# Optimization experiments

Measured on AMD Instinct MI355X. Metric: run time of the kernel, lower is better.

The kernel has to match this reference:

```python
import jax, jax.numpy as jnp
import numpy as np

B, T, D = 2, 2048, 1024
H = 16
HD = D // H  # head dim == config.k == config.v == 64


def setup_inputs() -> dict:
    key = jax.random.key(0)
    k1, k2, k3 = jax.random.split(key, 3)
    scale = 0.02
    x = jax.random.normal(k1, (B, T, D), dtype=jnp.float32)
    W1 = jax.random.normal(k2, (D, 3 * D), dtype=jnp.float32) * scale
    b1 = jnp.zeros((3 * D,), dtype=jnp.float32)
    W2 = jax.random.normal(k3, (D, D), dtype=jnp.float32) * scale
    b2 = jnp.zeros((D,), dtype=jnp.float32)
    return {"x": x, "W1": W1, "b1": b1, "W2": W2, "b2": b2}


def reference(x, W1, b1, W2, b2):
    # Fused QKV projection (dropout layers are identity in eval mode).
    Bx, Tx, C = x.shape
    qkv = x @ W1 + b1                      # [B, T, 3D]
    q, k, v = jnp.split(qkv, 3, axis=-1)   # each [B, T, D]
    q = q.reshape(Bx, Tx, H, HD).transpose(0, 2, 1, 3)  # [B, H, T, hd]
    k = k.reshape(Bx, Tx, H, HD).transpose(0, 2, 1, 3)
    v = v.reshape(Bx, Tx, H, HD).transpose(0, 2, 1, 3)

    logits = jnp.einsum('bhmk,bhnk->bhmn', q, k) / jnp.sqrt(jnp.float32(HD))
    # causal mask (lower-triangular bias buffer)
    causal = jnp.tril(jnp.ones((Tx, Tx), dtype=bool))
    logits = jnp.where(causal[None, None], logits, jnp.float32(-jnp.inf))
    att = jax.nn.softmax(logits, axis=-1)   # [B, H, T, T]

    y = jnp.einsum('bhmn,bhnv->bhmv', att, v)        # [B, H, T, hd]
    y = y.transpose(0, 2, 1, 3).reshape(Bx, Tx, C)   # [B, T, D]
    return y @ W2 + b2
```

## Files before the change

### kernel.cpp

```cpp
#include <hip/hip_runtime.h>

typedef __attribute__((ext_vector_type(8))) short bf16x8;
typedef __attribute__((ext_vector_type(4))) float f32x4;
typedef __attribute__((ext_vector_type(16))) float f32x16;
typedef __attribute__((ext_vector_type(4))) short short4v;
typedef __attribute__((ext_vector_type(4))) unsigned int uint4v;

#define B_  2
#define T_  2048
#define D_  1024
#define H_  16
#define HD_ 64

__device__ inline short f2bf(float f){
  unsigned u = __builtin_bit_cast(unsigned, f);
  u += 0x7fff + ((u >> 16) & 1);
  return (short)(u >> 16);
}
__device__ inline float bf2f(short s){
  unsigned u = ((unsigned)(unsigned short)s) << 16;
  return __builtin_bit_cast(float, u);
}

__device__ inline void gl2lds16(const void* g, void* l){
  __builtin_amdgcn_global_load_lds(
      (const __attribute__((address_space(1))) unsigned int*)g,
      (__attribute__((address_space(3))) unsigned int*)l, 16, 0, 0);
}

__device__ inline void transpose_tile(const float* __restrict__ in,
                                      short* __restrict__ out,
                                      int R, int C, int bx, int by){
  __shared__ float tile[32][33];
  int tx = threadIdx.x & 31, ty0 = threadIdx.x >> 5;
#pragma unroll
  for (int i = 0; i < 4; i++){
    int ty = ty0 + i * 8;
    tile[ty][tx] = in[(by + ty) * C + bx + tx];
  }
  __syncthreads();
#pragma unroll
  for (int i = 0; i < 4; i++){
    int ty = ty0 + i * 8;
    out[(bx + ty) * R + by + tx] = f2bf(tile[tx][ty]);
  }
}

__global__ __launch_bounds__(256) void prep(
    const float* __restrict__ x,  short* __restrict__ xb,
    const float* __restrict__ W1, short* __restrict__ W1T,
    const float* __restrict__ W2, short* __restrict__ W2T){
  const int bid = blockIdx.x;
  if (bid < 4096){
    int i = (bid * 256 + threadIdx.x) * 4;
    float4 v = *(const float4*)(x + i);
    short4v o;
    o[0] = f2bf(v.x); o[1] = f2bf(v.y); o[2] = f2bf(v.z); o[3] = f2bf(v.w);
    *(short4v*)(xb + i) = o;
  } else if (bid < 4096 + 3072){
    int tb = bid - 4096;
    transpose_tile(W1, W1T, 1024, 3072, (tb % 96) << 5, (tb / 96) << 5);
  } else {
    int tb = bid - 7168;
    transpose_tile(W2, W2T, 1024, 1024, (tb % 32) << 5, (tb / 32) << 5);
  }
}

#define QSCALE 0.18033688011112042f

__global__ __launch_bounds__(512) void gemm_qkv8(
    const short* __restrict__ A, const short* __restrict__ Bt,
    const float* __restrict__ bias,
    short* __restrict__ q, short* __restrict__ kk, short* __restrict__ vT){
  constexpr int K_ = 1024, NT = K_ / 64;
  __shared__ short As[2][256 * 64];
  __shared__ short Bs[2][192 * 64];
  const int tid = threadIdx.x;
  const int lane = tid & 63, w = tid >> 6;
  const int wm = w >> 2, wn = w & 3;
  const int lr = lane & 15, lk = lane >> 4;
  const int brow = blockIdx.y * 256, bcol = blockIdx.x * 192;
  const short* Ag = A  + brow * K_;
  const short* Bg = Bt + bcol * K_;
  f32x4 acc[8][3] = {};

  auto stageA = [&](int buf, int k0, int j){
    int idx = j * 512 + tid;
    int row = idx >> 3, cb = (idx & 7) * 16;
    int cs = cb ^ ((row & 7) << 4);
    gl2lds16(Ag + row * K_ + k0 + (cs >> 1), (char*)As[buf] + idx * 16);
  };
  auto stageB = [&](int buf, int k0, int j){
    int idx = j * 512 + tid;
    int row = idx >> 3, cb = (idx & 7) * 16;
    int cs = cb ^ ((row & 7) << 4);
    gl2lds16(Bg + row * K_ + k0 + (cs >> 1), (char*)Bs[buf] + idx * 16);
  };

#pragma unroll
  for (int j = 0; j < 4; j++) stageA(0, 0, j);
#pragma unroll
  for (int j = 0; j < 3; j++) stageB(0, 0, j);
  asm volatile("s_waitcnt vmcnt(0)" ::: "memory");
  __builtin_amdgcn_s_barrier();
  __builtin_amdgcn_sched_barrier(0);

  for (int t = 0; t < NT; ++t){
    const int cur = t & 1;
    const short* Ac = As[cur];
    const short* Bc = Bs[cur];
    const int nk0 = (t + 1) * 64;
    const bool pf = (t + 1 < NT);
    bf16x8 b[3][2];
#pragma unroll
    for (int p = 0; p < 4; p++){
      if (p == 0){
#pragma unroll
        for (int nf = 0; nf < 3; nf++){
          int rrow = wn * 48 + nf * 16 + lr;
          const char* rp = (const char*)Bc + rrow * 128;
          int swz = (rrow & 7) << 4;
#pragma unroll
          for (int kx = 0; kx < 2; kx++)
            b[nf][kx] = *(const bf16x8*)(rp + ((kx * 64 + lk * 16) ^ swz));
        }
      }
      bf16x8 a[2][2];
#pragma unroll
      for (int mf = 0; mf < 2; mf++){
        int arow = wm * 128 + p * 32 + mf * 16 + lr;
        const char* rp = (const char*)Ac + arow * 128;
        int swz = (arow & 7) << 4;
#pragma unroll
        for (int kx = 0; kx < 2; kx++)
          a[mf][kx] = *(const bf16x8*)(rp + ((kx * 64 + lk * 16) ^ swz));
      }
      if (pf){
        if (p == 0){ stageA(cur ^ 1, nk0, 0); stageA(cur ^ 1, nk0, 1); }
        else if (p == 1){ stageA(cur ^ 1, nk0, 2); stageA(cur ^ 1, nk0, 3); }
        else if (p == 2){ stageB(cur ^ 1, nk0, 0); stageB(cur ^ 1, nk0, 1); }
        else          {  stageB(cur ^ 1, nk0, 2); }
      }
      __builtin_amdgcn_sched_barrier(0);
      __builtin_amdgcn_s_barrier();
      __builtin_amdgcn_sched_barrier(0);
      __builtin_amdgcn_s_setprio(1);
#pragma unroll
      for (int mf = 0; mf < 2; mf++)
#pragma unroll
        for (int nf = 0; nf < 3; nf++)
#pragma unroll
          for (int kx = 0; kx < 2; kx++)
            acc[p * 2 + mf][nf] = __builtin_amdgcn_mfma_f32_16x16x32_bf16(
                a[mf][kx], b[nf][kx], acc[p * 2 + mf][nf], 0, 0, 0);
      __builtin_amdgcn_s_setprio(0);
      __builtin_amdgcn_sched_barrier(0);
      if (p == 3 && pf)
        asm volatile("s_waitcnt vmcnt(0)" ::: "memory");
      __builtin_amdgcn_s_barrier();
      __builtin_amdgcn_sched_barrier(0);
    }
  }

#pragma unroll
  for (int nf = 0; nf < 3; nf++){
    int n = bcol + wn * 48 + nf * 16 + lr;
    float bv = bias[n];
    int sec = n >> 10, d = n & 1023, h = d >> 6, hd = d & 63;
#pragma unroll
    for (int qd = 0; qd < 8; qd++){
      int m0 = brow + wm * 128 + qd * 16 + lk * 4;
      int bb = m0 >> 11, t0 = m0 & 2047;
      int bh = bb * H_ + h;
      if (sec == 0){
#pragma unroll
        for (int r = 0; r < 4; r++)
          q[(bh * T_ + t0 + r) * HD_ + hd] = f2bf((acc[qd][nf][r] + bv) * QSCALE);
      } else if (sec == 1){
#pragma unroll
        for (int r = 0; r < 4; r++)
          kk[(bh * T_ + t0 + r) * HD_ + hd] = f2bf(acc[qd][nf][r] + bv);
      } else {
        float v0 = acc[qd][nf][0] + bv, v1 = acc[qd][nf][1] + bv;
        float v2 = acc[qd][nf][2] + bv, v3 = acc[qd][nf][3] + bv;
        unsigned lo = (unsigned)(unsigned short)f2bf(v0) | ((unsigned)(unsigned short)f2bf(v1) << 16);
        unsigned hi = (unsigned)(unsigned short)f2bf(v2) | ((unsigned)(unsigned short)f2bf(v3) << 16);
        uint2 pk; pk.x = lo; pk.y = hi;
        *(uint2*)(vT + (bh * HD_ + hd) * T_ + t0) = pk;
      }
    }
  }
}

#define BM 128
#define BN 128
#define BK 32

template<int N_, int K_>
__global__ __launch_bounds__(256, 3) void gemm_bt(
    const short* __restrict__ A, const short* __restrict__ Bt,
    const float* __restrict__ bias, float* __restrict__ outf){
  __shared__ short As[3][BM * BK];
  __shared__ short Bs[3][BN * BK];
  const int tid = threadIdx.x;
  const int lane = tid & 63, w = tid >> 6;
  const int wm = w >> 1, wn = w & 1;
  const int lr = lane & 15, lk = lane >> 4;
  const int brow = blockIdx.y * BM, bcol = blockIdx.x * BN;
  f32x4 acc[4][4] = {};
  const short* Ag = A  + brow * K_;
  const short* Bg = Bt + bcol * K_;

  auto stage = [&](int buf, int k0){
#pragma unroll
    for (int i = 0; i < 2; i++){
      int idx = i * 256 + tid;
      int row = idx >> 2, c8 = (idx & 3) * 8;
      gl2lds16(Ag + row * K_ + k0 + c8, (char*)As[buf] + idx * 16);
      gl2lds16(Bg + row * K_ + k0 + c8, (char*)Bs[buf] + idx * 16);
    }
  };

  const int NT = K_ / BK;
  stage(0, 0);
  stage(1, BK);
  for (int t = 0; t < NT; ++t){
    if (t + 1 < NT)
      asm volatile("s_waitcnt vmcnt(4)" ::: "memory");
    else
      asm volatile("s_waitcnt vmcnt(0)" ::: "memory");
    __builtin_amdgcn_s_barrier();
    __builtin_amdgcn_sched_barrier(0);
    if (t + 2 < NT)
      stage((t + 2) % 3, (t + 2) * BK);
    __builtin_amdgcn_sched_barrier(0);

    const short* Ac = As[t % 3];
    const short* Bc = Bs[t % 3];
    bf16x8 a[4], b[4];
#pragma unroll
    for (int mf = 0; mf < 4; mf++)
      a[mf] = *(const bf16x8*)(Ac + (wm * 64 + mf * 16 + lr) * BK + lk * 8);
#pragma unroll
    for (int nf = 0; nf < 4; nf++)
      b[nf] = *(const bf16x8*)(Bc + (wn * 64 + nf * 16 + lr) * BK + lk * 8);
    __builtin_amdgcn_s_setprio(1);
#pragma unroll
    for (int mf = 0; mf < 4; mf++)
#pragma unroll
      for (int nf = 0; nf < 4; nf++)
        acc[mf][nf] = __builtin_amdgcn_mfma_f32_16x16x32_bf16(a[mf], b[nf], acc[mf][nf], 0, 0, 0);
    __builtin_amdgcn_s_setprio(0);
  }

#pragma unroll
  for (int nf = 0; nf < 4; nf++){
    int n = bcol + wn * 64 + nf * 16 + lr;
    float bv = bias[n];
#pragma unroll
    for (int mf = 0; mf < 4; mf++){
      int m0 = brow + wm * 64 + mf * 16 + lk * 4;
#pragma unroll
      for (int r = 0; r < 4; r++)
        outf[(m0 + r) * N_ + n] = acc[mf][nf][r] + bv;
    }
  }
}

__device__ inline int crow(int r, int h){ return (r & 3) + 8 * (r >> 2) + 4 * h; }

template<int NS>
__global__ __launch_bounds__(256, 4) void attn32(
    const short* __restrict__ Q, const short* __restrict__ Kg,
    const short* __restrict__ Vt, short* __restrict__ Y,
    short* __restrict__ Op, float* __restrict__ ml){
  __shared__ short Ks[2][64 * 64];
  __shared__ short Vs[2][64 * 64];
  __shared__ float bounce[4][32];
  const int tid = threadIdx.x;
  const int w = tid >> 6, l = tid & 63;
  const int lq = l & 31, h = l >> 5;
  const int bx = blockIdx.x;
  int i, hf;
  if constexpr (NS == 4){
    int u = bx >> 5, v = u & 15;
    i = (v < 8) ? 15 - v : v - 8;
    hf = u >> 4;
  } else {
    i = (bx < 256) ? 15 - (bx >> 5) : (bx >> 5) - 8;
    hf = 0;
  }
  const int bh = bx & 31;
  const int q0 = i * 128, qw = q0 + w * 32;
  const int nt = 2 * (i + 1);
  const int t0 = hf * nt / NS;
  const int t1 = (hf + 1) * nt / NS;

  bf16x8 qb[4];
  {
    const short* qbase = Q + (bh * T_ + qw + lq) * HD_;
#pragma unroll
    for (int dk = 0; dk < 4; dk++)
      qb[dk] = *(const bf16x8*)(qbase + dk * 16 + h * 8);
  }

  f32x16 o0 = {}, o1 = {};
  float m = -1e30f, ll = 0.f;

  auto stage = [&](int buf, int t){
#pragma unroll
    for (int j = 0; j < 2; j++){
      int idx = j * 256 + tid;
      int row = idx >> 3, cb = (idx & 7) * 16;
      int cbs = cb ^ ((row & 7) << 4);
      gl2lds16(Kg + (bh * T_ + t * 64 + row) * HD_ + (cbs >> 1), (char*)Ks[buf] + idx * 16);
      gl2lds16(Vt + (bh * HD_ + row) * T_ + t * 64 + (cbs >> 1), (char*)Vs[buf] + idx * 16);
    }
  };

  if (t0 < t1){
    stage(0, t0);
    for (int t = t0; t < t1; ++t){
      const int cur = (t - t0) & 1;
      if (t + 1 < t1){
        stage(cur ^ 1, t + 1);
        asm volatile("s_waitcnt vmcnt(4)" ::: "memory");
      } else {
        asm volatile("s_waitcnt vmcnt(0)" ::: "memory");
      }
      __builtin_amdgcn_s_barrier();
      __builtin_amdgcn_sched_barrier(0);

      const int kvb = t * 64;
      if (kvb <= qw + 31){
        const short* Kc = Ks[cur];
        const short* Vc = Vs[cur];

        f32x16 s[2] = {};
        __builtin_amdgcn_s_setprio(1);
#pragma unroll
        for (int kb = 0; kb < 2; kb++){
          int row = kb * 32 + lq;
          const char* rp = (const char*)Kc + row * 128;
          int swz = (row & 7) << 4;
#pragma unroll
          for (int dk = 0; dk < 4; dk++){
            bf16x8 ka = *(const bf16x8*)(rp + ((dk * 32 + h * 16) ^ swz));
            s[kb] = __builtin_amdgcn_mfma_f32_32x32x16_bf16(ka, qb[dk], s[kb], 0, 0, 0);
          }
        }
        __builtin_amdgcn_s_setprio(0);

        const int qg = qw + lq;
        if (kvb + 63 > qw){
#pragma unroll
          for (int kb = 0; kb < 2; kb++)
#pragma unroll
            for (int r = 0; r < 16; r++){
              int kv = kvb + kb * 32 + crow(r, h);
              if (kv > qg) s[kb][r] = -1e30f;
            }
        }

        float pm = s[0][0];
#pragma unroll
        for (int r = 1; r < 16; r++) pm = fmaxf(pm, s[0][r]);
#pragma unroll
        for (int r = 0; r < 16; r++) pm = fmaxf(pm, s[1][r]);
        pm = fmaxf(pm, __shfl_xor(pm, 32));

        if (__any(pm > m + 8.f)){
          float mn = fmaxf(pm, m);
          float sf = __builtin_amdgcn_exp2f(m - mn);
          m = mn;
          ll *= sf;
          bounce[w][lq] = sf;
#pragma unroll
          for (int r = 0; r < 16; r++){
            float sr = bounce[w][crow(r, h)];
            o0[r] *= sr; o1[r] *= sr;
          }
        }

        float ts = 0.f;
#pragma unroll
        for (int kb = 0; kb < 2; kb++)
#pragma unroll
          for (int r = 0; r < 16; r++){
            float p = __builtin_amdgcn_exp2f(s[kb][r] - m);
            s[kb][r] = p;
            ts += p;
          }
        ts += __shfl_xor(ts, 32);
        ll += ts;

        unsigned pw0[8], pw1[8];
#pragma unroll
        for (int kb = 0; kb < 2; kb++)
#pragma unroll
          for (int gg = 0; gg < 4; gg++){
            unsigned r0, r1;
            asm("v_cvt_pk_bf16_f32 %0, %1, %2" : "=v"(r0) : "v"(s[kb][gg * 4 + 0]), "v"(s[kb][gg * 4 + 1]));
            asm("v_cvt_pk_bf16_f32 %0, %1, %2" : "=v"(r1) : "v"(s[kb][gg * 4 + 2]), "v"(s[kb][gg * 4 + 3]));
            pw0[kb * 4 + gg] = r0;
            pw1[kb * 4 + gg] = r1;
          }
#pragma unroll
        for (int ks = 0; ks < 4; ks++){
          asm("v_permlane32_swap_b32 %0, %1" : "+v"(pw0[2 * ks]), "+v"(pw0[2 * ks + 1]));
          asm("v_permlane32_swap_b32 %0, %1" : "+v"(pw1[2 * ks]), "+v"(pw1[2 * ks + 1]));
        }

        __builtin_amdgcn_s_setprio(1);
#pragma unroll
        for (int ks = 0; ks < 4; ks++){
          uint4v paw;
          paw[0] = pw0[2 * ks];     paw[1] = pw1[2 * ks];
          paw[2] = pw0[2 * ks + 1]; paw[3] = pw1[2 * ks + 1];
          bf16x8 pa = __builtin_bit_cast(bf16x8, paw);
#pragma unroll
          for (int nb = 0; nb < 2; nb++){
            int row = nb * 32 + lq;
            bf16x8 vb = *(const bf16x8*)((const char*)Vc + row * 128 +
                          ((ks * 32 + h * 16) ^ ((row & 7) << 4)));
            if (nb == 0) o0 = __builtin_amdgcn_mfma_f32_32x32x16_bf16(pa, vb, o0, 0, 0, 0);
            else         o1 = __builtin_amdgcn_mfma_f32_32x32x16_bf16(pa, vb, o1, 0, 0, 0);
          }
        }
        __builtin_amdgcn_s_setprio(0);
      }
      __builtin_amdgcn_sched_barrier(0);
      __builtin_amdgcn_s_barrier();
    }
  }

  if constexpr (NS == 4){
    short* Oq = Op + ((size_t)(hf * 32 + bh)) * (size_t)T_ * 64;
    if (h == 0){
      float* mlr = ml + ((size_t)(hf * 32 + bh) * T_ + (qw + lq)) * 2;
      mlr[0] = m; mlr[1] = ll;
    }
#pragma unroll
    for (int r = 0; r < 16; r++){
      int qg = qw + crow(r, h);
      Oq[qg * 64 + lq]      = f2bf(o0[r]);
      Oq[qg * 64 + 32 + lq] = f2bf(o1[r]);
    }
  } else {
    bounce[w][lq] = __builtin_amdgcn_rcpf(ll);
    const int b = bh >> 4, hh = bh & 15;
#pragma unroll
    for (int r = 0; r < 16; r++){
      int row = crow(r, h);
      float rl = bounce[w][row];
      int qg = qw + row;
      short* yb = Y + (b * T_ + qg) * D_ + hh * 64;
      yb[lq]      = f2bf(o0[r] * rl);
      yb[32 + lq] = f2bf(o1[r] * rl);
    }
  }
}

__global__ __launch_bounds__(256) void attn_merge(
    const short* __restrict__ Op, const float* __restrict__ ml,
    short* __restrict__ Y){
  int gid = blockIdx.x * 256 + threadIdx.x;
  int rid = gid >> 2, c16 = (gid & 3) * 16;
  float mh[4], lh[4];
#pragma unroll
  for (int hf = 0; hf < 4; hf++){
    float2 v = *(const float2*)(ml + (size_t)hf * 131072 + rid * 2);
    mh[hf] = v.x; lh[hf] = v.y;
  }
  float M = fmaxf(fmaxf(mh[0], mh[1]), fmaxf(mh[2], mh[3]));
  float f[4], den = 0.f;
#pragma unroll
  for (int hf = 0; hf < 4; hf++){
    f[hf] = __builtin_amdgcn_exp2f(mh[hf] - M);
    den += f[hf] * lh[hf];
  }
  float rl = 1.f / den;
  float acc[16] = {};
#pragma unroll
  for (int hf = 0; hf < 4; hf++){
    const short* o = Op + (size_t)hf * 4194304 + (size_t)rid * 64 + c16;
    bf16x8 a = *(const bf16x8*)(o);
    bf16x8 b = *(const bf16x8*)(o + 8);
    float fh = f[hf];
#pragma unroll
    for (int j = 0; j < 8; j++){
      acc[j]     += fh * bf2f(a[j]);
      acc[8 + j] += fh * bf2f(b[j]);
    }
  }
  int bh = rid >> 11, t = rid & 2047;
  short* yb = Y + (((bh >> 4) * T_ + t) * D_) + (bh & 15) * 64 + c16;
  bf16x8 o0, o1;
#pragma unroll
  for (int j = 0; j < 8; j++){
    o0[j] = f2bf(acc[j] * rl);
    o1[j] = f2bf(acc[8 + j] * rl);
  }
  *(bf16x8*)(yb)     = o0;
  *(bf16x8*)(yb + 8) = o1;
}

extern "C" void kernel_launch(void* const* d_in, const int* in_sizes, int n_in,
                              void* d_out, int out_size, void* d_ws, size_t ws_size,
                              hipStream_t stream) {
  const float* x  = (const float*)d_in[0];
  const float* W1 = (const float*)d_in[1];
  const float* b1 = (const float*)d_in[2];
  const float* W2 = (const float*)d_in[3];
  const float* b2 = (const float*)d_in[4];
  float* out = (float*)d_out;

  char* ws = (char*)d_ws;
  short* W1T = (short*)(ws);
  short* W2T = (short*)(ws + 6291456);
  short* xb  = (short*)(ws + 8388608);
  short* q   = (short*)(ws + 16777216);
  short* kk  = (short*)(ws + 25165824);
  short* vT  = (short*)(ws + 33554432);
  short* Op  = (short*)(ws + 41943040);
  float* mlb = (float*)(ws);
  short* y   = xb;

  const size_t need = 41943040ull + 33554432ull;
  const bool split = ws_size >= need;

  prep<<<dim3(8192), dim3(256), 0, stream>>>(x, xb, W1, W1T, W2, W2T);
  gemm_qkv8<<<dim3(16, 16), dim3(512), 0, stream>>>(xb, W1T, b1, q, kk, vT);
  if (split){
    attn32<4><<<dim3(2048), dim3(256), 0, stream>>>(q, kk, vT, nullptr, Op, mlb);
    attn_merge<<<dim3(1024), dim3(256), 0, stream>>>(Op, mlb, y);
  } else {
    attn32<1><<<dim3(512), dim3(256), 0, stream>>>(q, kk, vT, y, nullptr, nullptr);
  }
  gemm_bt<1024, 1024><<<dim3(8, 32), dim3(256), 0, stream>>>(y, W2T, b2, out);
}
```

Baseline: 112.2 us.

## Enlarge QKV GEMM tile to 256x256 with four-phase LDS/MFMA interleaved schedule

The QKV projection GEMM now computes 256x256 output tiles instead of 256x192, dropping the grid from 16x16 to 12x16 blocks and raising arithmetic intensity per LDS load. The main loop is restructured into four quadrant sub-steps that interleave LDS fragment loads and global-to-LDS prefetch of the next K-tile with MFMA bursts, and each wave now stages its own rows. The goal is more data reuse and better overlap of memory with compute. In exchange, LDS use and accumulator registers grow, which may reduce occupancy, and 192 blocks may underfill the 256 CUs.

```diff
diff --git a/kernel.cpp b/kernel.cpp
--- a/kernel.cpp
+++ b/kernel.cpp
@@ -74,97 +74,113 @@
     short* __restrict__ q, short* __restrict__ kk, short* __restrict__ vT){
   constexpr int K_ = 1024, NT = K_ / 64;
   __shared__ short As[2][256 * 64];
-  __shared__ short Bs[2][192 * 64];
+  __shared__ short Bs[2][256 * 64];
   const int tid = threadIdx.x;
   const int lane = tid & 63, w = tid >> 6;
   const int wm = w >> 2, wn = w & 3;
   const int lr = lane & 15, lk = lane >> 4;
-  const int brow = blockIdx.y * 256, bcol = blockIdx.x * 192;
+  const int brow = blockIdx.y * 256, bcol = blockIdx.x * 256;
   const short* Ag = A  + brow * K_;
   const short* Bg = Bt + bcol * K_;
-  f32x4 acc[8][3] = {};
-
-  auto stageA = [&](int buf, int k0, int j){
-    int idx = j * 512 + tid;
-    int row = idx >> 3, cb = (idx & 7) * 16;
-    int cs = cb ^ ((row & 7) << 4);
-    gl2lds16(Ag + row * K_ + k0 + (cs >> 1), (char*)As[buf] + idx * 16);
+  f32x4 acc[8][4] = {};
+
+  auto stageA = [&](int buf, int k0){
+#pragma unroll
+    for (int j = 0; j < 4; j++){
+      int row = wm * 128 + wn * 32 + j * 8 + (lane >> 3);
+      int colb = (lane & 7) * 16;
+      int cs = colb ^ ((row & 7) << 4);
+      gl2lds16(Ag + row * K_ + k0 + (cs >> 1), (char*)As[buf] + row * 128 + colb);
+    }
   };
-  auto stageB = [&](int buf, int k0, int j){
-    int idx = j * 512 + tid;
-    int row = idx >> 3, cb = (idx & 7) * 16;
-    int cs = cb ^ ((row & 7) << 4);
-    gl2lds16(Bg + row * K_ + k0 + (cs >> 1), (char*)Bs[buf] + idx * 16);
+  auto stageB = [&](int buf, int k0){
+#pragma unroll
+    for (int j = 0; j < 4; j++){
+      int row = (wn >> 1) * 128 + (wm * 2 + (wn & 1)) * 32 + j * 8 + (lane >> 3);
+      int colb = (lane & 7) * 16;
+      int cs = colb ^ ((row & 7) << 4);
+      gl2lds16(Bg + row * K_ + k0 + (cs >> 1), (char*)Bs[buf] + row * 128 + colb);
+    }
   };
 
-#pragma unroll
-  for (int j = 0; j < 4; j++) stageA(0, 0, j);
-#pragma unroll
-  for (int j = 0; j < 3; j++) stageB(0, 0, j);
-  asm volatile("s_waitcnt vmcnt(0)" ::: "memory");
-  __builtin_amdgcn_s_barrier();
-  __builtin_amdgcn_sched_barrier(0);
+  bf16x8 aF[8], bF[4], bF2[4];
+  auto loadA = [&](const short* Ac, int r){
+#pragma unroll
+    for (int mf = 0; mf < 4; mf++){
+      int row = wm * 128 + r * 64 + mf * 16 + lr;
+      const char* rp = (const char*)Ac + row * 128;
+      int swz = (row & 7) << 4;
+#pragma unroll
+      for (int kx = 0; kx < 2; kx++)
+        aF[mf * 2 + kx] = *(const bf16x8*)(rp + ((kx * 64 + lk * 16) ^ swz));
+    }
+  };
+  auto loadB = [&](const short* Bc, int c, bf16x8* dst){
+#pragma unroll
+    for (int nf = 0; nf < 2; nf++){
+      int row = wn * 64 + c * 32 + nf * 16 + lr;
+      const char* rp = (const char*)Bc + row * 128;
+      int swz = (row & 7) << 4;
+#pragma unroll
+      for (int kx = 0; kx < 2; kx++)
+        dst[nf * 2 + kx] = *(const bf16x8*)(rp + ((kx * 64 + lk * 16) ^ swz));
+    }
+  };
+
+#define MFMA_SUB(r, c, B)                                                    \
+  __builtin_amdgcn_s_setprio(1);                                             \
+  _Pragma("unroll")                                                          \
+  for (int mf = 0; mf < 4; mf++)                                             \
+    _Pragma("unroll")                                                        \
+    for (int nf = 0; nf < 2; nf++)                                           \
+      _Pragma("unroll")                                                      \
+      for (int kx = 0; kx < 2; kx++)                                         \
+        acc[(r)*4 + mf][(c)*2 + nf] = __builtin_amdgcn_mfma_f32_16x16x32_bf16(\
+            aF[mf*2+kx], (B)[nf*2+kx], acc[(r)*4 + mf][(c)*2 + nf], 0, 0, 0);\
+  __builtin_amdgcn_s_setprio(0);
+
+  stageA(0, 0);
+  stageB(0, 0);
 
   for (int t = 0; t < NT; ++t){
-    const int cur = t & 1;
+    const int cur = t & 1, nxt = cur ^ 1;
     const short* Ac = As[cur];
     const short* Bc = Bs[cur];
-    const int nk0 = (t + 1) * 64;
     const bool pf = (t + 1 < NT);
-    bf16x8 b[3][2];
-#pragma unroll
-    for (int p = 0; p < 4; p++){
-      if (p == 0){
-#pragma unroll
-        for (int nf = 0; nf < 3; nf++){
-          int rrow = wn * 48 + nf * 16 + lr;
-          const char* rp = (const char*)Bc + rrow * 128;
-          int swz = (rrow & 7) << 4;
-#pragma unroll
-          for (int kx = 0; kx < 2; kx++)
-            b[nf][kx] = *(const bf16x8*)(rp + ((kx * 64 + lk * 16) ^ swz));
-        }
-      }
-      bf16x8 a[2][2];
-#pragma unroll
-      for (int mf = 0; mf < 2; mf++){
-        int arow = wm * 128 + p * 32 + mf * 16 + lr;
-        const char* rp = (const char*)Ac + arow * 128;
-        int swz = (arow & 7) << 4;
-#pragma unroll
-        for (int kx = 0; kx < 2; kx++)
-          a[mf][kx] = *(const bf16x8*)(rp + ((kx * 64 + lk * 16) ^ swz));
-      }
-      if (pf){
-        if (p == 0){ stageA(cur ^ 1, nk0, 0); stageA(cur ^ 1, nk0, 1); }
-        else if (p == 1){ stageA(cur ^ 1, nk0, 2); stageA(cur ^ 1, nk0, 3); }
-        else if (p == 2){ stageB(cur ^ 1, nk0, 0); stageB(cur ^ 1, nk0, 1); }
-        else          {  stageB(cur ^ 1, nk0, 2); }
-      }
-      __builtin_amdgcn_sched_barrier(0);
-      __builtin_amdgcn_s_barrier();
-      __builtin_amdgcn_sched_barrier(0);
-      __builtin_amdgcn_s_setprio(1);
-#pragma unroll
-      for (int mf = 0; mf < 2; mf++)
-#pragma unroll
-        for (int nf = 0; nf < 3; nf++)
-#pragma unroll
-          for (int kx = 0; kx < 2; kx++)
-            acc[p * 2 + mf][nf] = __builtin_amdgcn_mfma_f32_16x16x32_bf16(
-                a[mf][kx], b[nf][kx], acc[p * 2 + mf][nf], 0, 0, 0);
-      __builtin_amdgcn_s_setprio(0);
-      __builtin_amdgcn_sched_barrier(0);
-      if (p == 3 && pf)
-        asm volatile("s_waitcnt vmcnt(0)" ::: "memory");
-      __builtin_amdgcn_s_barrier();
-      __builtin_amdgcn_sched_barrier(0);
-    }
-  }
-
-#pragma unroll
-  for (int nf = 0; nf < 3; nf++){
-    int n = bcol + wn * 48 + nf * 16 + lr;
+    asm volatile("s_waitcnt vmcnt(0)" ::: "memory");
+    __builtin_amdgcn_s_barrier();
+    __builtin_amdgcn_sched_barrier(0);
+    loadA(Ac, 0);
+    loadB(Bc, 0, bF);
+    if (pf) stageA(nxt, (t + 1) * 64);
+    __builtin_amdgcn_sched_barrier(0);
+    __builtin_amdgcn_s_barrier();
+    __builtin_amdgcn_sched_barrier(0);
+    MFMA_SUB(0, 0, bF)
+    __builtin_amdgcn_sched_barrier(0);
+    __builtin_amdgcn_s_barrier();
+    loadB(Bc, 1, bF2);
+    if (pf) stageB(nxt, (t + 1) * 64);
+    __builtin_amdgcn_sched_barrier(0);
+    __builtin_amdgcn_s_barrier();
+    __builtin_amdgcn_sched_barrier(0);
+    MFMA_SUB(0, 1, bF2)
+    __builtin_amdgcn_sched_barrier(0);
+    __builtin_amdgcn_s_barrier();
+    loadA(Ac, 1);
+    __builtin_amdgcn_sched_barrier(0);
+    __builtin_amdgcn_s_barrier();
+    __builtin_amdgcn_sched_barrier(0);
+    MFMA_SUB(1, 0, bF)
+    __builtin_amdgcn_sched_barrier(0);
+    __builtin_amdgcn_s_barrier();
+    MFMA_SUB(1, 1, bF2)
+    __builtin_amdgcn_sched_barrier(0);
+  }
+
+#pragma unroll
+  for (int nf = 0; nf < 4; nf++){
+    int n = bcol + wn * 64 + nf * 16 + lr;
     float bv = bias[n];
     int sec = n >> 10, d = n & 1023, h = d >> 6, hd = d & 63;
 #pragma unroll
@@ -530,7 +546,7 @@
   const bool split = ws_size >= need;
 
   prep<<<dim3(8192), dim3(256), 0, stream>>>(x, xb, W1, W1T, W2, W2T);
-  gemm_qkv8<<<dim3(16, 16), dim3(512), 0, stream>>>(xb, W1T, b1, q, kk, vT);
+  gemm_qkv8<<<dim3(12, 16), dim3(512), 0, stream>>>(xb, W1T, b1, q, kk, vT);
   if (split){
     attn32<4><<<dim3(2048), dim3(256), 0, stream>>>(q, kk, vT, nullptr, Op, mlb);
     attn_merge<<<dim3(1024), dim3(256), 0, stream>>>(Op, mlb, y);
```

Result: slower. 114.9 us (+2.4%).
